# Kernel optimization log

Measured on AMD Instinct MI355X. Metric: run time of the kernel, lower is better.

Reference implementation:

```python
import jax, jax.numpy as jnp
import numpy as np

B, L, D, H = 2, 2048, 2048, 16
HD = D // H  # 128, must be even for RoPE


def rope(x, seq_len, theta=10000.0):
    """Apply RoPE to x of shape [B, H, L, Dh]."""
    d = x.shape[-1]
    freqs = 1.0 / theta ** (jnp.arange(0, d, 2, dtype=x.dtype) / d)  # [d/2]
    t = jnp.arange(seq_len, dtype=x.dtype)
    f = jnp.outer(t, freqs)                      # [L, d/2]
    sin = jnp.repeat(jnp.sin(f), 2, axis=-1)     # [L, d]
    cos = jnp.repeat(jnp.cos(f), 2, axis=-1)
    x1, x2 = x[..., ::2], x[..., 1::2]
    x_rot = jnp.stack([-x2, x1], axis=-1).reshape(x.shape)
    return x * cos + x_rot * sin


def setup_inputs() -> dict:
    key = jax.random.key(0)
    k1, k2, k3 = jax.random.split(key, 3)
    x = jax.random.normal(k1, (B, L, D), dtype=jnp.float32)
    w_qkv = jax.random.normal(k2, (D, 3 * D), dtype=jnp.float32) * (1.0 / np.sqrt(D))
    w_proj = jax.random.normal(k3, (D, D), dtype=jnp.float32) * (1.0 / np.sqrt(D))
    return {"x": x, "w_qkv": w_qkv, "w_proj": w_proj}


def reference(x, w_qkv, w_proj):
    Bc, Lc, Dc = x.shape
    scale = 1.0 / np.sqrt(HD)
    qkv = (x @ w_qkv).reshape(Bc, Lc, 3, H, HD)
    q, k, v = qkv[:, :, 0], qkv[:, :, 1], qkv[:, :, 2]   # [B, L, H, Dh]
    # transpose to [B, H, L, Dh], then RoPE (position axis = L)
    q = rope(jnp.transpose(q, (0, 2, 1, 3)), Lc)
    k = rope(jnp.transpose(k, (0, 2, 1, 3)), Lc)
    v = jnp.transpose(v, (0, 2, 1, 3))
    att = jnp.einsum("bhqd,bhkd->bhqk", q, k) * scale   # [B, H, L, L]
    att = jax.nn.softmax(att, axis=-1)
    out = jnp.einsum("bhqk,bhkd->bhqd", att, v)          # [B, H, L, Dh]
    out = jnp.transpose(out, (0, 2, 1, 3)).reshape(Bc, Lc, Dc)
    return out @ w_proj
```

## Files before the change

kernel.cpp:

```cpp
#include <hip/hip_runtime.h>
#include <hip/hip_bf16.h>
#include <cstdint>

typedef short short8 __attribute__((ext_vector_type(8)));
typedef float f32x4 __attribute__((ext_vector_type(4)));
typedef float f32x16 __attribute__((ext_vector_type(16)));
typedef int i32x4 __attribute__((ext_vector_type(4)));

#define AS1 __attribute__((address_space(1)))
#define AS3 __attribute__((address_space(3)))

static __device__ __forceinline__ void async_cp16(const void* g, void* l) {
  __builtin_amdgcn_global_load_lds((const AS1 unsigned int*)g, (AS3 unsigned int*)l, 16, 0, 0);
}

static __device__ __forceinline__ ushort f2bf(float f) {
  unsigned u = __builtin_bit_cast(unsigned, f);
  u += 0x7fffu + ((u >> 16) & 1u);
  return (ushort)(u >> 16);
}
static __device__ __forceinline__ float bf2f(ushort h) {
  unsigned u = ((unsigned)h) << 16;
  return __builtin_bit_cast(float, u);
}

#define FENCE asm volatile("" ::: "memory")
#define BARRIER do { FENCE; __builtin_amdgcn_s_barrier(); FENCE; } while (0)
#define WAITLGKM asm volatile("s_waitcnt lgkmcnt(0)" ::: "memory")
#define WAITVM(N) asm volatile("s_waitcnt vmcnt(" #N ")" ::: "memory")

__global__ void cvt_bf16_kernel(const float* __restrict__ in, ushort* __restrict__ out, int n4) {
  int i = blockIdx.x * blockDim.x + threadIdx.x;
  if (i >= n4) return;
  float4 v = ((const float4*)in)[i];
  ushort4 o;
  o.x = f2bf(v.x); o.y = f2bf(v.y); o.z = f2bf(v.z); o.w = f2bf(v.w);
  ((ushort4*)out)[i] = o;
}

__global__ void transpose_cvt_kernel(const float* __restrict__ in, ushort* __restrict__ out,
                                     int R, int C) {
  __shared__ ushort tile[32][33];
  int c0 = blockIdx.x * 32, r0 = blockIdx.y * 32;
  int tx = threadIdx.x, ty = threadIdx.y;
  for (int j = 0; j < 32; j += 8)
    tile[ty + j][tx] = f2bf(in[(size_t)(r0 + ty + j) * C + c0 + tx]);
  __syncthreads();
  for (int j = 0; j < 32; j += 8)
    out[(size_t)(c0 + ty + j) * R + r0 + tx] = tile[tx][ty + j];
}

__global__ void rope_tab_kernel(float2* __restrict__ tab) {
  int idx = blockIdx.x * 256 + threadIdx.x;
  int i = idx & 63, l = idx >> 6;
  float inv = __builtin_amdgcn_exp2f(-(float)i * (13.287712379549449f / 64.0f));
  float f = (float)l * inv;
  float s, c;
  sincosf(f, &s, &c);
  tab[idx] = make_float2(c, s);
}

__global__ __launch_bounds__(512, 2) void gemm_qkv_kernel(
    const ushort* __restrict__ A, const ushort* __restrict__ Bt,
    ushort* __restrict__ qr, ushort* __restrict__ kr, ushort* __restrict__ vt,
    const float2* __restrict__ rtab, int K, int N) {
  __shared__ __align__(16) ushort smem[65536];
  const int tid = threadIdx.x;
  const int wave = tid >> 6, lane = tid & 63;
  const int wm = wave >> 2, wn = wave & 3;
  const int m0 = blockIdx.y * 256, n0 = blockIdx.x * 256;
  const int frl = lane & 15, fq = lane >> 4;
  const int sx = fq ^ (frl & 7);
  const int srow = tid >> 3;
  const int slog8 = (((tid & 7) ^ ((tid >> 3) & 7)) << 3);

  const ushort* aG = A + (size_t)(m0 + srow) * K + slog8;
  const ushort* bG = Bt + (size_t)(n0 + srow) * K + slog8;
  ushort* lw = smem + wave * 512;

  f32x4 acc[8][4] = {};
  short8 aF[4][2], bF[2][2][2];

  auto stA = [&](int tt, int h) {
    ushort* l = lw + (tt & 1) * 32768 + h * 8192;
    const ushort* g = aG + (size_t)(h * 128) * K + tt * 64;
    async_cp16(g, l);
    async_cp16(g + (size_t)64 * K, l + 4096);
  };
  auto stB = [&](int tt, int h) {
    ushort* l = lw + (tt & 1) * 32768 + 16384 + h * 8192;
    const ushort* g = bG + (size_t)(h * 128) * K + tt * 64;
    async_cp16(g, l);
    async_cp16(g + (size_t)64 * K, l + 4096);
  };
  auto LDA = [&](int buf, int mh) {
#pragma unroll
    for (int mf = 0; mf < 4; ++mf)
#pragma unroll
      for (int kk = 0; kk < 2; ++kk)
        aF[mf][kk] = *(const short8*)(smem + buf * 32768 +
            (wm * 128 + mh * 64 + mf * 16 + frl) * 64 + ((sx ^ (kk << 2)) << 3));
  };
  auto LDB = [&](int buf, int nh) {
#pragma unroll
    for (int j = 0; j < 2; ++j)
#pragma unroll
      for (int kk = 0; kk < 2; ++kk)
        bF[nh][j][kk] = *(const short8*)(smem + buf * 32768 + 16384 +
            (wn * 64 + nh * 32 + j * 16 + frl) * 64 + ((sx ^ (kk << 2)) << 3));
  };
  auto MFMAQ = [&](int mh, int nh) {
    __builtin_amdgcn_s_setprio(1);
#pragma unroll
    for (int mf = 0; mf < 4; ++mf)
#pragma unroll
      for (int j = 0; j < 2; ++j)
#pragma unroll
        for (int kk = 0; kk < 2; ++kk)
          acc[mh * 4 + mf][nh * 2 + j] = __builtin_amdgcn_mfma_f32_16x16x32_bf16(
              aF[mf][kk], bF[nh][j][kk], acc[mh * 4 + mf][nh * 2 + j], 0, 0, 0);
    __builtin_amdgcn_s_setprio(0);
  };

  stB(0, 0); stB(0, 1); stA(0, 0); stA(0, 1);
  stB(1, 0); stB(1, 1);
  WAITVM(4);
  BARRIER;

  const int NT = K >> 6;
  for (int i = 0; i < NT / 2 - 1; ++i) {
    const int t = 2 * i;
    LDA(0, 0); LDB(0, 0); stA(t + 1, 0);
    BARRIER; WAITLGKM; MFMAQ(0, 0); BARRIER;
    LDB(0, 1); stA(t + 1, 1);
    BARRIER; WAITLGKM; MFMAQ(0, 1); BARRIER;
    LDA(0, 1); stB(t + 2, 0);
    BARRIER; WAITLGKM; MFMAQ(1, 0); BARRIER;
    stB(t + 2, 1);
    BARRIER; WAITLGKM; MFMAQ(1, 1); WAITVM(4); BARRIER;
    LDA(1, 0); LDB(1, 0); stA(t + 2, 0);
    BARRIER; WAITLGKM; MFMAQ(0, 0); BARRIER;
    LDB(1, 1); stA(t + 2, 1);
    BARRIER; WAITLGKM; MFMAQ(0, 1); BARRIER;
    LDA(1, 1); stB(t + 3, 0);
    BARRIER; WAITLGKM; MFMAQ(1, 0); BARRIER;
    stB(t + 3, 1);
    BARRIER; WAITLGKM; MFMAQ(1, 1); WAITVM(4); BARRIER;
  }
  {
    const int t = NT - 2;
    LDA(0, 0); LDB(0, 0); stA(t + 1, 0);
    BARRIER; WAITLGKM; MFMAQ(0, 0); BARRIER;
    LDB(0, 1); stA(t + 1, 1);
    BARRIER; WAITLGKM; MFMAQ(0, 1); BARRIER;
    LDA(0, 1);
    BARRIER; WAITLGKM; MFMAQ(1, 0); BARRIER;
    BARRIER; WAITLGKM; MFMAQ(1, 1); WAITVM(0); BARRIER;
    LDA(1, 0); LDB(1, 0);
    BARRIER; WAITLGKM; MFMAQ(0, 0); BARRIER;
    LDB(1, 1);
    BARRIER; WAITLGKM; MFMAQ(0, 1); BARRIER;
    LDA(1, 1);
    BARRIER; WAITLGKM; MFMAQ(1, 0); BARRIER;
    BARRIER; WAITLGKM; MFMAQ(1, 1); BARRIER;
  }

  const int rq = fq * 4;
  if (n0 < 4096) {
    ushort* dst = (n0 >= 2048) ? kr : qr;
#pragma unroll
    for (int mi = 0; mi < 8; ++mi)
#pragma unroll
      for (int ni = 0; ni < 4; ++ni) {
        int col = n0 + wn * 64 + ni * 16 + frl;
        int rem = col & 2047, h = rem >> 7, dh = rem & 127;
        int ip = dh >> 1;
        float sgn = (dh & 1) ? 1.0f : -1.0f;
#pragma unroll
        for (int r = 0; r < 4; ++r) {
          int row = m0 + wm * 128 + mi * 16 + rq + r;
          int b = row >> 11, l = row & 2047;
          float v = acc[mi][ni][r];
          float vp = __shfl_xor(v, 1);
          float2 cs2 = rtab[l * 64 + ip];
          float o = v * cs2.x + sgn * vp * cs2.y;
          dst[((size_t)((b << 4) + h) * 2048 + l) * 128 + dh] = f2bf(o);
        }
      }
  } else {
    ushort* vtile = smem + wave * 1024;
    const int col0 = n0 + wn * 64;
    const int row0 = m0 + wm * 128;
    const int b = row0 >> 11, l0 = row0 & 2047;
    const int swz = (frl & 3) << 4;
#pragma unroll
    for (int hm = 0; hm < 2; ++hm)
#pragma unroll
      for (int ni = 0; ni < 4; ++ni) {
#pragma unroll
        for (int mi = 0; mi < 4; ++mi)
#pragma unroll
          for (int r = 0; r < 4; ++r) {
            int ll = mi * 16 + rq + r;
            vtile[frl * 64 + (ll ^ swz)] = f2bf(acc[hm * 4 + mi][ni][r]);
          }
#pragma unroll
        for (int tt = 0; tt < 2; ++tt) {
          int dl = tt * 8 + (lane >> 3);
          int l8 = (lane & 7) * 8;
          int lsw = l8 ^ ((dl & 3) << 4);
          int rem = (col0 + ni * 16 + dl) & 2047;
          int h = rem >> 7, dh = rem & 127;
          *(short8*)(vt + ((size_t)((b << 4) + h) * 128 + dh) * 2048 + l0 + hm * 64 + l8) =
              *(const short8*)(vtile + dl * 64 + lsw);
        }
      }
  }
}

__global__ __launch_bounds__(512, 2) void gemm_out_kernel(
    const ushort* __restrict__ A, const ushort* __restrict__ Bt,
    float* __restrict__ C, int K, int N) {
  __shared__ __align__(16) ushort smem[49152];
  const int tid = threadIdx.x;
  const int wave = tid >> 6, lane = tid & 63;
  const int wm = wave >> 2, wn = wave & 3;
  const int m0 = blockIdx.y * 128, n0 = blockIdx.x * 256;
  const int frl = lane & 15, fq = lane >> 4;
  const int sx = fq ^ (frl & 7);
  const int srow = tid >> 3;
  const int slog8 = (((tid & 7) ^ ((tid >> 3) & 7)) << 3);

  const ushort* aG = A + (size_t)(m0 + srow) * K + slog8;
  const ushort* bG = Bt + (size_t)(n0 + srow) * K + slog8;
  ushort* lw = smem + wave * 512;

  f32x4 acc[4][4] = {};
  short8 aF[2][2], bF[2][2][2];

  auto stA = [&](int tt) {
    ushort* l = lw + (tt & 1) * 24576;
    const ushort* g = aG + tt * 64;
    async_cp16(g, l);
    async_cp16(g + (size_t)64 * K, l + 4096);
  };
  auto stB = [&](int tt, int h) {
    ushort* l = lw + (tt & 1) * 24576 + 8192 + h * 8192;
    const ushort* g = bG + (size_t)(h * 128) * K + tt * 64;
    async_cp16(g, l);
    async_cp16(g + (size_t)64 * K, l + 4096);
  };
  auto LDA = [&](int buf, int mh) {
#pragma unroll
    for (int mf = 0; mf < 2; ++mf)
#pragma unroll
      for (int kk = 0; kk < 2; ++kk)
        aF[mf][kk] = *(const short8*)(smem + buf * 24576 +
            (wm * 64 + mh * 32 + mf * 16 + frl) * 64 + ((sx ^ (kk << 2)) << 3));
  };
  auto LDB = [&](int buf, int nh) {
#pragma unroll
    for (int j = 0; j < 2; ++j)
#pragma unroll
      for (int kk = 0; kk < 2; ++kk)
        bF[nh][j][kk] = *(const short8*)(smem + buf * 24576 + 8192 +
            (wn * 64 + nh * 32 + j * 16 + frl) * 64 + ((sx ^ (kk << 2)) << 3));
  };
  auto MFMAQ = [&](int mh, int nh) {
    __builtin_amdgcn_s_setprio(1);
#pragma unroll
    for (int mf = 0; mf < 2; ++mf)
#pragma unroll
      for (int j = 0; j < 2; ++j)
#pragma unroll
        for (int kk = 0; kk < 2; ++kk)
          acc[mh * 2 + mf][nh * 2 + j] = __builtin_amdgcn_mfma_f32_16x16x32_bf16(
              aF[mf][kk], bF[nh][j][kk], acc[mh * 2 + mf][nh * 2 + j], 0, 0, 0);
    __builtin_amdgcn_s_setprio(0);
  };

  stB(0, 0); stB(0, 1); stA(0);
  stB(1, 0); stB(1, 1);
  WAITVM(4);
  BARRIER;

  const int NT = K >> 6;
  for (int i = 0; i < NT / 2 - 1; ++i) {
    const int t = 2 * i;
    LDA(0, 0); LDB(0, 0); stA(t + 1);
    BARRIER; WAITLGKM; MFMAQ(0, 0); BARRIER;
    LDB(0, 1);
    BARRIER; WAITLGKM; MFMAQ(0, 1); BARRIER;
    LDA(0, 1); stB(t + 2, 0);
    BARRIER; WAITLGKM; MFMAQ(1, 0); BARRIER;
    stB(t + 2, 1);
    BARRIER; WAITLGKM; MFMAQ(1, 1); WAITVM(4); BARRIER;
    LDA(1, 0); LDB(1, 0); stA(t + 2);
    BARRIER; WAITLGKM; MFMAQ(0, 0); BARRIER;
    LDB(1, 1);
    BARRIER; WAITLGKM; MFMAQ(0, 1); BARRIER;
    LDA(1, 1); stB(t + 3, 0);
    BARRIER; WAITLGKM; MFMAQ(1, 0); BARRIER;
    stB(t + 3, 1);
    BARRIER; WAITLGKM; MFMAQ(1, 1); WAITVM(4); BARRIER;
  }
  {
    const int t = NT - 2;
    LDA(0, 0); LDB(0, 0); stA(t + 1);
    BARRIER; WAITLGKM; MFMAQ(0, 0); BARRIER;
    LDB(0, 1);
    BARRIER; WAITLGKM; MFMAQ(0, 1); BARRIER;
    LDA(0, 1);
    BARRIER; WAITLGKM; MFMAQ(1, 0); BARRIER;
    BARRIER; WAITLGKM; MFMAQ(1, 1); WAITVM(0); BARRIER;
    LDA(1, 0); LDB(1, 0);
    BARRIER; WAITLGKM; MFMAQ(0, 0); BARRIER;
    LDB(1, 1);
    BARRIER; WAITLGKM; MFMAQ(0, 1); BARRIER;
    LDA(1, 1);
    BARRIER; WAITLGKM; MFMAQ(1, 0); BARRIER;
    BARRIER; WAITLGKM; MFMAQ(1, 1); BARRIER;
  }

  const int rq = fq * 4;
#pragma unroll
  for (int mi = 0; mi < 4; ++mi)
#pragma unroll
    for (int nj = 0; nj < 4; ++nj) {
      int col = n0 + wn * 64 + nj * 16 + frl;
#pragma unroll
      for (int r = 0; r < 4; ++r) {
        int row = m0 + wm * 64 + mi * 16 + rq + r;
        C[(size_t)row * N + col] = acc[mi][nj][r];
      }
    }
}

__global__ __launch_bounds__(512, 2) void flash_kernel(
    const ushort* __restrict__ qr, const ushort* __restrict__ kr,
    const ushort* __restrict__ vtg, ushort* __restrict__ att) {
  __shared__ __align__(16) ushort KV[2][16384];

  const int tid = threadIdx.x;
  const int wave = tid >> 6, lane = tid & 63;
  const int bid = blockIdx.x;
  const int swzb = (bid & 7) * 32 + (bid >> 3);
  const int qt = swzb & 7;
  const int bh = swzb >> 3;
  const int q0 = qt * 256 + wave * 32;
  const size_t bh_base = (size_t)bh * 2048 * 128;

  const int qi = lane & 31, hi = lane >> 5;
  const float cs = 0.08838834764831845f * 1.4426950408889634f;
  const int rsw = (qi & 7) << 3;

  const int krow0 = wave * 8 + (lane >> 4);
  const int kgc = (lane & 15) * 8;
  const int vrow0 = wave * 16 + (lane >> 3);
  const int vgc = (lane & 7) * 8;

  auto stage = [&](int kt, int buf) {
#pragma unroll
    for (int i = 0; i < 2; ++i) {
      const int krow = krow0 + i * 4;
      async_cp16(kr + bh_base + (size_t)(kt * 64 + krow) * 128 + (kgc ^ ((krow & 7) << 3)),
                 &KV[buf][(wave * 2 + i) * 512]);
      const int vrow = vrow0 + i * 8;
      async_cp16(vtg + bh_base + (size_t)vrow * 2048 + kt * 64 + (vgc ^ ((vrow & 7) << 3)),
                 &KV[buf][8192 + (wave * 2 + i) * 512]);
    }
  };

  short8 qf[8];
  {
    const ushort* qp = qr + bh_base + (size_t)(q0 + qi) * 128 + hi * 8;
#pragma unroll
    for (int c = 0; c < 8; ++c) qf[c] = *(const short8*)(qp + c * 16);
  }

  f32x16 oacc[4];
#pragma unroll
  for (int nt = 0; nt < 4; ++nt)
#pragma unroll
    for (int r = 0; r < 16; ++r) oacc[nt][r] = 0.f;
  float l_lane = 0.f;

  stage(0, 0);
  stage(1, 1);
  WAITVM(4);
  BARRIER;

#pragma unroll 2
  for (int kt = 0; kt < 32; ++kt) {
    const int bo = (kt & 1) * 16384;
    const ushort* kv = &KV[0][0];

    f32x16 s0, s1;
#pragma unroll
    for (int r = 0; r < 16; ++r) { s0[r] = 0.f; s1[r] = 0.f; }
    const ushort* kp0 = kv + bo + (size_t)(0 * 32 + qi) * 128;
    const ushort* kp1 = kv + bo + (size_t)(1 * 32 + qi) * 128;
    __builtin_amdgcn_s_setprio(1);
#pragma unroll
    for (int c = 0; c < 8; ++c) {
      const int co = (c * 16 + hi * 8) ^ rsw;
      short8 kf0 = *(const short8*)(kp0 + co);
      short8 kf1 = *(const short8*)(kp1 + co);
      s0 = __builtin_amdgcn_mfma_f32_32x32x16_bf16(kf0, qf[c], s0, 0, 0, 0);
      s1 = __builtin_amdgcn_mfma_f32_32x32x16_bf16(kf1, qf[c], s1, 0, 0, 0);
    }
    __builtin_amdgcn_s_setprio(0);

    int pk[2][8];
#pragma unroll
    for (int m = 0; m < 8; ++m) {
      float a0 = __builtin_amdgcn_exp2f(s0[2 * m] * cs);
      float a1 = __builtin_amdgcn_exp2f(s0[2 * m + 1] * cs);
      float b0 = __builtin_amdgcn_exp2f(s1[2 * m] * cs);
      float b1 = __builtin_amdgcn_exp2f(s1[2 * m + 1] * cs);
      l_lane += (a0 + a1) + (b0 + b1);
      pk[0][m] = (int)f2bf(a0) | ((int)f2bf(a1) << 16);
      pk[1][m] = (int)f2bf(b0) | ((int)f2bf(b1) << 16);
    }

    __builtin_amdgcn_s_setprio(1);
#pragma unroll
    for (int ks = 0; ks < 4; ++ks) {
      const int kb = ks >> 1, s2 = ks & 1;
      const int a0 = pk[kb][4 * s2 + 0], a1 = pk[kb][4 * s2 + 1];
      const int a2 = pk[kb][4 * s2 + 2], a3 = pk[kb][4 * s2 + 3];
      const int p0 = __shfl_xor(a0, 32), p1 = __shfl_xor(a1, 32);
      const int p2 = __shfl_xor(a2, 32), p3 = __shfl_xor(a3, 32);
      i32x4 w;
      w[0] = hi ? p2 : a0;
      w[1] = hi ? p3 : a1;
      w[2] = hi ? a2 : p0;
      w[3] = hi ? a3 : p1;
      short8 pa = __builtin_bit_cast(short8, w);
      const int vco = (ks * 16 + hi * 8) ^ rsw;
#pragma unroll
      for (int nt = 0; nt < 4; ++nt) {
        short8 vf = *(const short8*)(kv + bo + 8192 + (size_t)(nt * 32 + qi) * 64 + vco);
        oacc[nt] = __builtin_amdgcn_mfma_f32_32x32x16_bf16(pa, vf, oacc[nt], 0, 0, 0);
      }
    }
    __builtin_amdgcn_s_setprio(0);

    BARRIER;
    if (kt < 30) {
      stage(kt + 2, kt & 1);
      WAITVM(4);
    } else {
      WAITVM(0);
    }
    BARRIER;
  }

  l_lane += __shfl_xor(l_lane, 32);
  const float linv = 1.0f / l_lane;
  const int b = bh >> 4, h = bh & 15;
#pragma unroll
  for (int r = 0; r < 16; ++r) {
    const int crow = (r & 3) + 8 * (r >> 2) + 4 * hi;
    const float inv = __shfl(linv, crow);
    const size_t rowa = (size_t)(b * 2048 + q0 + crow) * 2048 + h * 128;
#pragma unroll
    for (int nt = 0; nt < 4; ++nt)
      att[rowa + nt * 32 + qi] = f2bf(oacc[nt][r] * inv);
  }
}

extern "C" void kernel_launch(void* const* d_in, const int* in_sizes, int n_in,
                              void* d_out, int out_size, void* d_ws, size_t ws_size,
                              hipStream_t stream) {
  const float* x = (const float*)d_in[0];
  const float* w_qkv = (const float*)d_in[1];
  const float* w_proj = (const float*)d_in[2];
  float* out = (float*)d_out;

  char* p = (char*)d_ws;
  ushort* xb = (ushort*)p;  p += (size_t)4096 * 2048 * 2;
  ushort* wqt = (ushort*)p; p += (size_t)6144 * 2048 * 2;
  ushort* wpt = (ushort*)p; p += (size_t)2048 * 2048 * 2;
  ushort* qr = (ushort*)p;  p += (size_t)32 * 2048 * 128 * 2;
  ushort* kr = (ushort*)p;  p += (size_t)32 * 2048 * 128 * 2;
  ushort* vt = (ushort*)p;  p += (size_t)32 * 2048 * 128 * 2;
  ushort* att = (ushort*)p; p += (size_t)4096 * 2048 * 2;
  float2* rtab = (float2*)p; p += (size_t)2048 * 64 * 8;

  rope_tab_kernel<<<512, 256, 0, stream>>>(rtab);
  cvt_bf16_kernel<<<8192, 256, 0, stream>>>(x, xb, 4096 * 2048 / 4);
  transpose_cvt_kernel<<<dim3(192, 64), dim3(32, 8), 0, stream>>>(w_qkv, wqt, 2048, 6144);
  transpose_cvt_kernel<<<dim3(64, 64), dim3(32, 8), 0, stream>>>(w_proj, wpt, 2048, 2048);
  gemm_qkv_kernel<<<dim3(24, 16), 512, 0, stream>>>(xb, wqt, qr, kr, vt, rtab, 2048, 6144);
  flash_kernel<<<256, 512, 0, stream>>>(qr, kr, vt, att);
  gemm_out_kernel<<<dim3(8, 32), 512, 0, stream>>>(att, wpt, out, 2048, 2048);
}
```

Baseline: 391.8 us.

## Merge preprocessing kernels into one launch and coarsen GEMM pipeline phases

Four preprocessing launches (x convert, RoPE table, two weight transpose-converts) are merged into one kernel that picks its job from the block index. The transpose store now writes ushort2 pairs instead of single ushorts. In the GEMM main loop (the one whose epilogue writes C; its kernel header is not shown) the k-step phases go from four MFMA quarters to two halves, halving the barriers per step. The larger phases need more B fragments live at once, which may raise register pressure and give less overlap between LDS loads and MFMAs.

```diff
diff --git a/kernel.cpp b/kernel.cpp
--- a/kernel.cpp
+++ b/kernel.cpp
@@ -29,35 +29,53 @@
 #define WAITLGKM asm volatile("s_waitcnt lgkmcnt(0)" ::: "memory")
 #define WAITVM(N) asm volatile("s_waitcnt vmcnt(" #N ")" ::: "memory")
 
-__global__ void cvt_bf16_kernel(const float* __restrict__ in, ushort* __restrict__ out, int n4) {
-  int i = blockIdx.x * blockDim.x + threadIdx.x;
-  if (i >= n4) return;
-  float4 v = ((const float4*)in)[i];
-  ushort4 o;
-  o.x = f2bf(v.x); o.y = f2bf(v.y); o.z = f2bf(v.z); o.w = f2bf(v.w);
-  ((ushort4*)out)[i] = o;
-}
-
-__global__ void transpose_cvt_kernel(const float* __restrict__ in, ushort* __restrict__ out,
-                                     int R, int C) {
-  __shared__ ushort tile[32][33];
-  int c0 = blockIdx.x * 32, r0 = blockIdx.y * 32;
-  int tx = threadIdx.x, ty = threadIdx.y;
-  for (int j = 0; j < 32; j += 8)
-    tile[ty + j][tx] = f2bf(in[(size_t)(r0 + ty + j) * C + c0 + tx]);
-  __syncthreads();
-  for (int j = 0; j < 32; j += 8)
-    out[(size_t)(c0 + ty + j) * R + r0 + tx] = tile[tx][ty + j];
-}
-
-__global__ void rope_tab_kernel(float2* __restrict__ tab) {
-  int idx = blockIdx.x * 256 + threadIdx.x;
-  int i = idx & 63, l = idx >> 6;
-  float inv = __builtin_amdgcn_exp2f(-(float)i * (13.287712379549449f / 64.0f));
-  float f = (float)l * inv;
-  float s, c;
-  sincosf(f, &s, &c);
-  tab[idx] = make_float2(c, s);
+__global__ __launch_bounds__(256) void prepro_kernel(
+    const float* __restrict__ x, const float* __restrict__ w_qkv,
+    const float* __restrict__ w_proj, ushort* __restrict__ xb,
+    ushort* __restrict__ wqt, ushort* __restrict__ wpt, float2* __restrict__ rtab) {
+  const int bid = blockIdx.x;
+  const int tid = threadIdx.x;
+  if (bid < 8192) {
+    int i = bid * 256 + tid;
+    float4 v = ((const float4*)x)[i];
+    ushort4 o;
+    o.x = f2bf(v.x); o.y = f2bf(v.y); o.z = f2bf(v.z); o.w = f2bf(v.w);
+    ((ushort4*)xb)[i] = o;
+  } else if (bid < 8704) {
+    int idx = (bid - 8192) * 256 + tid;
+    int i = idx & 63, l = idx >> 6;
+    float inv = __builtin_amdgcn_exp2f(-(float)i * (13.287712379549449f / 64.0f));
+    float f = (float)l * inv;
+    float s, c;
+    sincosf(f, &s, &c);
+    rtab[idx] = make_float2(c, s);
+  } else {
+    const float* in;
+    ushort* out;
+    int R, C, bx, by;
+    if (bid < 8704 + 12288) {
+      int tb = bid - 8704;
+      in = w_qkv; out = wqt; R = 2048; C = 6144; bx = tb % 192; by = tb / 192;
+    } else {
+      int tb = bid - 20992;
+      in = w_proj; out = wpt; R = 2048; C = 2048; bx = tb % 64; by = tb / 64;
+    }
+    __shared__ ushort tile[32][33];
+    int c0 = bx * 32, r0 = by * 32;
+    int tx = tid & 31, ty = tid >> 5;
+    for (int j = 0; j < 32; j += 8)
+      tile[ty + j][tx] = f2bf(in[(size_t)(r0 + ty + j) * C + c0 + tx]);
+    __syncthreads();
+    int u = tid & 15;
+#pragma unroll
+    for (int jj = 0; jj < 2; ++jj) {
+      int rowc = (tid >> 4) + jj * 16;
+      ushort2 o2;
+      o2.x = tile[2 * u][rowc];
+      o2.y = tile[2 * u + 1][rowc];
+      *(ushort2*)(out + (size_t)(c0 + rowc) * R + r0 + 2 * u) = o2;
+    }
+  }
 }
 
 __global__ __launch_bounds__(512, 2) void gemm_qkv_kernel(
@@ -266,16 +284,18 @@
         bF[nh][j][kk] = *(const short8*)(smem + buf * 24576 + 8192 +
             (wn * 64 + nh * 32 + j * 16 + frl) * 64 + ((sx ^ (kk << 2)) << 3));
   };
-  auto MFMAQ = [&](int mh, int nh) {
+  auto MFMAH = [&](int mh) {
     __builtin_amdgcn_s_setprio(1);
 #pragma unroll
     for (int mf = 0; mf < 2; ++mf)
 #pragma unroll
-      for (int j = 0; j < 2; ++j)
-#pragma unroll
-        for (int kk = 0; kk < 2; ++kk)
-          acc[mh * 2 + mf][nh * 2 + j] = __builtin_amdgcn_mfma_f32_16x16x32_bf16(
-              aF[mf][kk], bF[nh][j][kk], acc[mh * 2 + mf][nh * 2 + j], 0, 0, 0);
+      for (int nh = 0; nh < 2; ++nh)
+#pragma unroll
+        for (int j = 0; j < 2; ++j)
+#pragma unroll
+          for (int kk = 0; kk < 2; ++kk)
+            acc[mh * 2 + mf][nh * 2 + j] = __builtin_amdgcn_mfma_f32_16x16x32_bf16(
+                aF[mf][kk], bF[nh][j][kk], acc[mh * 2 + mf][nh * 2 + j], 0, 0, 0);
     __builtin_amdgcn_s_setprio(0);
   };
 
@@ -287,39 +307,25 @@
   const int NT = K >> 6;
   for (int i = 0; i < NT / 2 - 1; ++i) {
     const int t = 2 * i;
-    LDA(0, 0); LDB(0, 0); stA(t + 1);
-    BARRIER; WAITLGKM; MFMAQ(0, 0); BARRIER;
-    LDB(0, 1);
-    BARRIER; WAITLGKM; MFMAQ(0, 1); BARRIER;
-    LDA(0, 1); stB(t + 2, 0);
-    BARRIER; WAITLGKM; MFMAQ(1, 0); BARRIER;
-    stB(t + 2, 1);
-    BARRIER; WAITLGKM; MFMAQ(1, 1); WAITVM(4); BARRIER;
-    LDA(1, 0); LDB(1, 0); stA(t + 2);
-    BARRIER; WAITLGKM; MFMAQ(0, 0); BARRIER;
-    LDB(1, 1);
-    BARRIER; WAITLGKM; MFMAQ(0, 1); BARRIER;
-    LDA(1, 1); stB(t + 3, 0);
-    BARRIER; WAITLGKM; MFMAQ(1, 0); BARRIER;
-    stB(t + 3, 1);
-    BARRIER; WAITLGKM; MFMAQ(1, 1); WAITVM(4); BARRIER;
+    LDA(0, 0); LDB(0, 0); LDB(0, 1); stA(t + 1);
+    BARRIER; WAITLGKM; MFMAH(0); BARRIER;
+    LDA(0, 1); stB(t + 2, 0); stB(t + 2, 1);
+    BARRIER; WAITLGKM; MFMAH(1); WAITVM(4); BARRIER;
+    LDA(1, 0); LDB(1, 0); LDB(1, 1); stA(t + 2);
+    BARRIER; WAITLGKM; MFMAH(0); BARRIER;
+    LDA(1, 1); stB(t + 3, 0); stB(t + 3, 1);
+    BARRIER; WAITLGKM; MFMAH(1); WAITVM(4); BARRIER;
   }
   {
     const int t = NT - 2;
-    LDA(0, 0); LDB(0, 0); stA(t + 1);
-    BARRIER; WAITLGKM; MFMAQ(0, 0); BARRIER;
-    LDB(0, 1);
-    BARRIER; WAITLGKM; MFMAQ(0, 1); BARRIER;
+    LDA(0, 0); LDB(0, 0); LDB(0, 1); stA(t + 1);
+    BARRIER; WAITLGKM; MFMAH(0); BARRIER;
     LDA(0, 1);
-    BARRIER; WAITLGKM; MFMAQ(1, 0); BARRIER;
-    BARRIER; WAITLGKM; MFMAQ(1, 1); WAITVM(0); BARRIER;
-    LDA(1, 0); LDB(1, 0);
-    BARRIER; WAITLGKM; MFMAQ(0, 0); BARRIER;
-    LDB(1, 1);
-    BARRIER; WAITLGKM; MFMAQ(0, 1); BARRIER;
+    BARRIER; WAITLGKM; MFMAH(1); WAITVM(0); BARRIER;
+    LDA(1, 0); LDB(1, 0); LDB(1, 1);
+    BARRIER; WAITLGKM; MFMAH(0); BARRIER;
     LDA(1, 1);
-    BARRIER; WAITLGKM; MFMAQ(1, 0); BARRIER;
-    BARRIER; WAITLGKM; MFMAQ(1, 1); BARRIER;
+    BARRIER; WAITLGKM; MFMAH(1); BARRIER;
   }
 
   const int rq = fq * 4;
@@ -488,10 +494,7 @@
   ushort* att = (ushort*)p; p += (size_t)4096 * 2048 * 2;
   float2* rtab = (float2*)p; p += (size_t)2048 * 64 * 8;
 
-  rope_tab_kernel<<<512, 256, 0, stream>>>(rtab);
-  cvt_bf16_kernel<<<8192, 256, 0, stream>>>(x, xb, 4096 * 2048 / 4);
-  transpose_cvt_kernel<<<dim3(192, 64), dim3(32, 8), 0, stream>>>(w_qkv, wqt, 2048, 6144);
-  transpose_cvt_kernel<<<dim3(64, 64), dim3(32, 8), 0, stream>>>(w_proj, wpt, 2048, 2048);
+  prepro_kernel<<<25088, 256, 0, stream>>>(x, w_qkv, w_proj, xb, wqt, wpt, rtab);
   gemm_qkv_kernel<<<dim3(24, 16), 512, 0, stream>>>(xb, wqt, qr, kr, vt, rtab, 2048, 6144);
   flash_kernel<<<256, 512, 0, stream>>>(qr, kr, vt, att);
   gemm_out_kernel<<<dim3(8, 32), 512, 0, stream>>>(att, wpt, out, 2048, 2048);
```

Result: faster. 380.8 us (-2.8%).
